# Optimization experiments

Measured on AMD Instinct MI355X. Metric: run time of the kernel, lower is better.

## Reference

```python
import jax, jax.numpy as jnp
import numpy as np

BN_EPS = 1e-5

def _bn(h, g, b):
    # BatchNorm1d training-mode math: biased batch stats over the node axis.
    m = h.mean(axis=0)
    v = h.var(axis=0)
    return (h - m) * jax.lax.rsqrt(v + BN_EPS) * g + b

def setup_inputs() -> dict:
    key = jax.random.key(0)
    ks = jax.random.split(key, 8)
    N, E, D_IN, H, L = 50000, 800000, 128, 256, 3
    return {
        "x": jax.random.normal(ks[0], (N, D_IN), dtype=jnp.float32),
        "edge_index": jax.random.randint(ks[1], (2, E), 0, N, dtype=jnp.int64),
        "eps": jnp.zeros((L,), dtype=jnp.float32),
        "W1_0": jax.random.normal(ks[2], (D_IN, H), dtype=jnp.float32),
        "W1_rest": jax.random.normal(ks[3], (L - 1, H, H), dtype=jnp.float32),
        "b1": jnp.zeros((L, H), dtype=jnp.float32),
        "g1": jnp.ones((L, H), dtype=jnp.float32),
        "bt1": jnp.zeros((L, H), dtype=jnp.float32),
        "W2": jax.random.normal(ks[4], (L, H, H), dtype=jnp.float32),
        "b2": jnp.zeros((L, H), dtype=jnp.float32),
        "g2": jnp.ones((L, H), dtype=jnp.float32),
        "bt2": jnp.zeros((L, H), dtype=jnp.float32),
    }

def reference(x, edge_index, eps, W1_0, W1_rest, b1, g1, bt1, W2, b2, g2, bt2):
    N = x.shape[0]
    row, col = edge_index[0], edge_index[1]
    L = eps.shape[0]

    def gin_layer(h, eps_i, Wa, ba, ga, bta, Wb, bb, gb, btb):
        # sum_{u in N(v)} h_u : gather source feats, scatter-add to dest rows
        agg = jax.ops.segment_sum(h[col], row, num_segments=N)
        out = (1.0 + eps_i) * h + agg
        out = _bn(out @ Wa + ba, ga, bta)        # Linear -> BN
        out = jax.nn.relu(out)                    # ReLU
        out = _bn(out @ Wb + bb, gb, btb)        # Linear -> BN
        return out

    h = x
    for i in range(L):
        Wa = W1_0 if i == 0 else W1_rest[i - 1]
        h = gin_layer(h, eps[i], Wa, b1[i], g1[i], bt1[i], W2[i], b2[i], g2[i], bt2[i])
        if i < L - 1:
            h = jax.nn.relu(h)  # inter-layer ReLU; dropout is identity in eval mode
    return h
```

## Files before the change

### kernel.cpp

```cpp
#include <hip/hip_runtime.h>
#include <hip/hip_bf16.h>
#include <math.h>
#include <stdint.h>

typedef short short8 __attribute__((ext_vector_type(8)));
typedef float f32x4 __attribute__((ext_vector_type(4)));

__device__ __forceinline__ float bf2f(unsigned int u) {
    union { unsigned int i; float f; } x; x.i = u << 16; return x.f;
}
__device__ __forceinline__ unsigned short f2bf(float f) {
    union { float f; unsigned int i; } x; x.f = f;
    unsigned int r = x.i + 0x7fffu + ((x.i >> 16) & 1u);
    return (unsigned short)(r >> 16);
}

__global__ void block_sums(const int* __restrict__ deg, int* __restrict__ bs, int N) {
    __shared__ int tmp[256];
    int t = threadIdx.x;
    int i = blockIdx.x * 256 + t;
    tmp[t] = (i < N) ? deg[i] : 0;
    __syncthreads();
    for (int off = 128; off > 0; off >>= 1) {
        if (t < off) tmp[t] += tmp[t + off];
        __syncthreads();
    }
    if (t == 0) bs[blockIdx.x] = tmp[0];
}
__global__ void scan_bs(const int* __restrict__ bs, int* __restrict__ bo, int B) {
    __shared__ int tmp[256];
    int t = threadIdx.x;
    int v = (t < B) ? bs[t] : 0;
    tmp[t] = v;
    __syncthreads();
    for (int off = 1; off < 256; off <<= 1) {
        int x = (t >= off) ? tmp[t - off] : 0;
        __syncthreads();
        tmp[t] += x;
        __syncthreads();
    }
    bo[t] = tmp[t] - v;
}
__global__ void finalize_rowptr(const int* __restrict__ deg, const int* __restrict__ bo,
                                int* __restrict__ rowptr, int* __restrict__ cursor,
                                int N, int E) {
    __shared__ int tmp[256];
    int t = threadIdx.x;
    int i = blockIdx.x * 256 + t;
    int v = (i < N) ? deg[i] : 0;
    tmp[t] = v;
    __syncthreads();
    for (int off = 1; off < 256; off <<= 1) {
        int x = (t >= off) ? tmp[t - off] : 0;
        __syncthreads();
        tmp[t] += x;
        __syncthreads();
    }
    int excl = tmp[t] - v + bo[blockIdx.x];
    if (i < N) { rowptr[i] = excl; cursor[i] = excl; }
    if (i == N) rowptr[N] = E;
}
__global__ void fill_csr(const int* __restrict__ row, const int* __restrict__ col,
                         int* __restrict__ cursor, int* __restrict__ idx, int E) {
    int e = blockIdx.x * blockDim.x + threadIdx.x;
    if (e < E) {
        int p = atomicAdd(&cursor[row[e]], 1);
        idx[p] = col[e];
    }
}

__global__ void zero_all(int* __restrict__ deg, int n_deg,
                         uint4* __restrict__ a, uint4* __restrict__ b, uint4* __restrict__ c,
                         int n_t, uint4* __restrict__ st, int n_st) {
    int i = blockIdx.x * blockDim.x + threadIdx.x;
    uint4 z = make_uint4(0, 0, 0, 0);
    if (i < n_deg) deg[i] = 0;
    if (i < n_t) { a[i] = z; b[i] = z; c[i] = z; }
    if (i < n_st) st[i] = z;
}

__global__ void prep_all(const float* __restrict__ x, unsigned short* __restrict__ xb, int nconv,
                         const float* __restrict__ W1_0, const float* __restrict__ W1rest,
                         const float* __restrict__ W2, unsigned short* __restrict__ wt,
                         const int* __restrict__ erow, int* __restrict__ deg, int E) {
    int i = blockIdx.x * blockDim.x + threadIdx.x;
    if (i < nconv) {
        float4 v = *(const float4*)(x + (size_t)i * 4);
        unsigned int lo = (unsigned int)f2bf(v.x) | ((unsigned int)f2bf(v.y) << 16);
        unsigned int hi = (unsigned int)f2bf(v.z) | ((unsigned int)f2bf(v.w) << 16);
        *(uint2*)(xb + (size_t)i * 4) = make_uint2(lo, hi);
        return;
    }
    int id = i - nconv;
    if (id < 32768) {
        int k = id >> 8, c = id & 255;
        wt[c * 128 + k] = f2bf(W1_0[id]);
        return;
    } else if (id < 163840) {
        int t = id - 32768;
        int m = t >> 16, r = t & 65535;
        int k = r >> 8, c = r & 255;
        wt[32768 + m * 65536 + c * 256 + k] = f2bf(W1rest[t]);
        return;
    } else if (id < 360448) {
        int t = id - 163840;
        int m = t >> 16, r = t & 65535;
        int k = r >> 8, c = r & 255;
        wt[163840 + m * 65536 + c * 256 + k] = f2bf(W2[t]);
        return;
    }
    int e = id - 360448;
    if (e < E) atomicAdd(&deg[erow[e]], 1);
}

template<int H, bool FUSE_BN>
__global__ __launch_bounds__(256) void aggregate_f(
    const unsigned short* __restrict__ h,
    const int* __restrict__ rowptr, const int* __restrict__ idx,
    const float* __restrict__ eps_p, int layer,
    const float* __restrict__ stats, const float* __restrict__ g,
    const float* __restrict__ bt, float invN,
    unsigned short* __restrict__ out, int N) {
    constexpr int NW = H / 128;
    int lane = threadIdx.x & 63;
    int v = blockIdx.x * 4 + (threadIdx.x >> 6);
    if (v >= N) return;

    float sc[2 * NW], sh[2 * NW];
    if constexpr (FUSE_BN) {
#pragma unroll
        for (int j = 0; j < 2 * NW; ++j) {
            int c = lane * 2 * NW + j;
            float m = stats[c] * invN;
            float var = stats[256 + c] * invN - m * m;
            sc[j] = g[c] * rsqrtf(var + 1e-5f);
            sh[j] = bt[c] - m * sc[j];
        }
    }
    const float s = 1.f + eps_p[layer];
    const unsigned int* hu = (const unsigned int*)h;

    float acc[2 * NW];
    {
        const unsigned int* hv = hu + (size_t)v * (H / 2) + lane * NW;
#pragma unroll
        for (int j = 0; j < NW; ++j) {
            unsigned int r = hv[j];
            float f0 = bf2f(r & 0xffffu), f1 = bf2f(r >> 16);
            if constexpr (FUSE_BN) {
                f0 = fmaxf(f0 * sc[2 * j] + sh[2 * j], 0.f);
                f1 = fmaxf(f1 * sc[2 * j + 1] + sh[2 * j + 1], 0.f);
            }
            acc[2 * j] = s * f0;
            acc[2 * j + 1] = s * f1;
        }
    }
    int e = rowptr[v], end = rowptr[v + 1];
    for (; e + 3 < end; e += 4) {
        int u0 = idx[e], u1 = idx[e + 1], u2 = idx[e + 2], u3 = idx[e + 3];
        const unsigned int* q0 = hu + (size_t)u0 * (H / 2) + lane * NW;
        const unsigned int* q1 = hu + (size_t)u1 * (H / 2) + lane * NW;
        const unsigned int* q2 = hu + (size_t)u2 * (H / 2) + lane * NW;
        const unsigned int* q3 = hu + (size_t)u3 * (H / 2) + lane * NW;
        unsigned int r0[NW], r1[NW], r2[NW], r3[NW];
#pragma unroll
        for (int j = 0; j < NW; ++j) { r0[j] = q0[j]; r1[j] = q1[j]; r2[j] = q2[j]; r3[j] = q3[j]; }
#pragma unroll
        for (int j = 0; j < NW; ++j) {
            float a0 = bf2f(r0[j] & 0xffffu), b0 = bf2f(r0[j] >> 16);
            float a1 = bf2f(r1[j] & 0xffffu), b1 = bf2f(r1[j] >> 16);
            float a2 = bf2f(r2[j] & 0xffffu), b2 = bf2f(r2[j] >> 16);
            float a3 = bf2f(r3[j] & 0xffffu), b3 = bf2f(r3[j] >> 16);
            if constexpr (FUSE_BN) {
                float c0 = sc[2 * j], d0 = sh[2 * j], c1 = sc[2 * j + 1], d1 = sh[2 * j + 1];
                a0 = fmaxf(a0 * c0 + d0, 0.f); b0 = fmaxf(b0 * c1 + d1, 0.f);
                a1 = fmaxf(a1 * c0 + d0, 0.f); b1 = fmaxf(b1 * c1 + d1, 0.f);
                a2 = fmaxf(a2 * c0 + d0, 0.f); b2 = fmaxf(b2 * c1 + d1, 0.f);
                a3 = fmaxf(a3 * c0 + d0, 0.f); b3 = fmaxf(b3 * c1 + d1, 0.f);
            }
            acc[2 * j]     += (a0 + a1) + (a2 + a3);
            acc[2 * j + 1] += (b0 + b1) + (b2 + b3);
        }
    }
    for (; e < end; ++e) {
        const unsigned int* q = hu + (size_t)idx[e] * (H / 2) + lane * NW;
#pragma unroll
        for (int j = 0; j < NW; ++j) {
            unsigned int r = q[j];
            float f0 = bf2f(r & 0xffffu), f1 = bf2f(r >> 16);
            if constexpr (FUSE_BN) {
                f0 = fmaxf(f0 * sc[2 * j] + sh[2 * j], 0.f);
                f1 = fmaxf(f1 * sc[2 * j + 1] + sh[2 * j + 1], 0.f);
            }
            acc[2 * j] += f0;
            acc[2 * j + 1] += f1;
        }
    }
    unsigned int* op = (unsigned int*)out + (size_t)v * (H / 2) + lane * NW;
#pragma unroll
    for (int j = 0; j < NW; ++j)
        op[j] = (unsigned int)f2bf(acc[2 * j]) | ((unsigned int)f2bf(acc[2 * j + 1]) << 16);
}

template<int K, bool TRANS_A>
__global__ __launch_bounds__(512, 4) void gemm_mfma(const unsigned short* __restrict__ A,
                                                 const unsigned short* __restrict__ Wt,
                                                 const float* __restrict__ bias,
                                                 const float* __restrict__ stats_in,
                                                 const float* __restrict__ gp,
                                                 const float* __restrict__ btp,
                                                 float invN,
                                                 unsigned short* __restrict__ Y,
                                                 float* __restrict__ stats_out,
                                                 int Nrows) {
    __shared__ unsigned short sA[2][128 * 32];
    __shared__ unsigned short sB[2][256 * 32];
    __shared__ float reds[256], redq[256];
    __shared__ float spc[256], sps[256];
    const int tid = threadIdx.x;
    const int lane = tid & 63;
    const int wid = tid >> 6;
    const int wm = wid >> 2;
    const int wn = wid & 3;
    const int r0 = blockIdx.x * 128;
    const int arow = tid >> 2;
    const int akk = (((tid & 3) ^ ((tid >> 3) & 3))) * 8;

    if constexpr (TRANS_A) {
        if (tid < 256) {
            float m = stats_in[tid] * invN;
            float var = stats_in[256 + tid] * invN - m * m;
            float sv = gp[tid] * rsqrtf(var + 1e-5f);
            spc[tid] = sv;
            sps[tid] = btp[tid] - m * sv;
        }
        __syncthreads();
    }

    f32x4 acc[4][4] = {};

    auto stageB = [&](int buf, int k0) {
#pragma unroll
        for (int q = 0; q < 2; ++q) {
            int row = q * 128 + arow;
            const unsigned short* gB = Wt + (size_t)row * K + k0 + akk;
            __builtin_amdgcn_global_load_lds(
                (const __attribute__((address_space(1))) void*)(uintptr_t)gB,
                (__attribute__((address_space(3))) void*)(uintptr_t)(&sB[buf][q * 4096 + tid * 8]),
                16, 0, 0);
        }
    };
    auto stageA_direct = [&](int buf, int k0) {
        const unsigned short* gA = A + (size_t)(r0 + arow) * K + k0 + akk;
        __builtin_amdgcn_global_load_lds(
            (const __attribute__((address_space(1))) void*)(uintptr_t)gA,
            (__attribute__((address_space(3))) void*)(uintptr_t)(&sA[buf][tid * 8]),
            16, 0, 0);
    };
    uint4 areg;
    auto loadA = [&](int k0) {
        areg = *(const uint4*)(A + (size_t)(r0 + arow) * K + k0 + akk);
    };
    auto writeA = [&](int buf, int k0) {
        float4 sca = *(const float4*)&spc[k0 + akk];
        float4 scb = *(const float4*)&spc[k0 + akk + 4];
        float4 sha = *(const float4*)&sps[k0 + akk];
        float4 shb = *(const float4*)&sps[k0 + akk + 4];
        uint4 u = areg;
        float f0 = fmaxf(bf2f(u.x & 0xffffu) * sca.x + sha.x, 0.f);
        float f1 = fmaxf(bf2f(u.x >> 16)     * sca.y + sha.y, 0.f);
        float f2 = fmaxf(bf2f(u.y & 0xffffu) * sca.z + sha.z, 0.f);
        float f3 = fmaxf(bf2f(u.y >> 16)     * sca.w + sha.w, 0.f);
        float f4 = fmaxf(bf2f(u.z & 0xffffu) * scb.x + shb.x, 0.f);
        float f5 = fmaxf(bf2f(u.z >> 16)     * scb.y + shb.y, 0.f);
        float f6 = fmaxf(bf2f(u.w & 0xffffu) * scb.z + shb.z, 0.f);
        float f7 = fmaxf(bf2f(u.w >> 16)     * scb.w + shb.w, 0.f);
        uint4 w;
        w.x = (unsigned int)f2bf(f0) | ((unsigned int)f2bf(f1) << 16);
        w.y = (unsigned int)f2bf(f2) | ((unsigned int)f2bf(f3) << 16);
        w.z = (unsigned int)f2bf(f4) | ((unsigned int)f2bf(f5) << 16);
        w.w = (unsigned int)f2bf(f6) | ((unsigned int)f2bf(f7) << 16);
        *(uint4*)&sA[buf][tid * 8] = w;
    };

    const int nt = K / 32;
    if constexpr (TRANS_A) { loadA(0); } else { stageA_direct(0, 0); }
    stageB(0, 0);
    const int krow = lane >> 4;
    const int rl = lane & 15;
    const int ksw = (rl >> 1) & 3;

    for (int t = 0; t < nt; ++t) {
        if constexpr (TRANS_A) writeA(t & 1, t * 32);
        __syncthreads();
        if (t + 1 < nt) {
            stageB((t + 1) & 1, (t + 1) * 32);
            if constexpr (TRANS_A) loadA((t + 1) * 32);
            else stageA_direct((t + 1) & 1, (t + 1) * 32);
        }
        const unsigned short* sAb = sA[t & 1];
        const unsigned short* sBb = sB[t & 1];
        short8 a[4], b[4];
#pragma unroll
        for (int i = 0; i < 4; ++i) {
            a[i] = *(const short8*)(sAb + (wm * 64 + i * 16 + rl) * 32 + (krow ^ ksw) * 8);
            b[i] = *(const short8*)(sBb + (wn * 64 + i * 16 + rl) * 32 + (krow ^ ksw) * 8);
        }
#pragma unroll
        for (int i = 0; i < 4; ++i)
#pragma unroll
            for (int n = 0; n < 4; ++n)
                asm volatile("v_mfma_f32_16x16x32_bf16 %0, %1, %2, %0"
                             : "+v"(acc[i][n])
                             : "v"(a[i]), "v"(b[n]));
    }
    asm volatile("s_nop 7\n\ts_nop 7" ::);

    const int rg = lane >> 4;
    float ssum[4], qsum[4];
#pragma unroll
    for (int n = 0; n < 4; ++n) {
        int col = wn * 64 + n * 16 + rl;
        float bvv = bias[col];
        float s = 0.f, q2 = 0.f;
#pragma unroll
        for (int i = 0; i < 4; ++i) {
#pragma unroll
            for (int r = 0; r < 4; ++r) {
                int grow = r0 + wm * 64 + i * 16 + rg * 4 + r;
                if (grow < Nrows) {
                    float v = acc[i][n][r] + bvv;
                    Y[(size_t)grow * 256 + col] = f2bf(v);
                    s += v;
                    q2 += v * v;
                }
            }
        }
        s  += __shfl_xor(s, 16, 64);  s  += __shfl_xor(s, 32, 64);
        q2 += __shfl_xor(q2, 16, 64); q2 += __shfl_xor(q2, 32, 64);
        ssum[n] = s; qsum[n] = q2;
    }
    if (wm == 0 && rg == 0) {
#pragma unroll
        for (int n = 0; n < 4; ++n) {
            int lc = wn * 64 + n * 16 + rl;
            reds[lc] = ssum[n];
            redq[lc] = qsum[n];
        }
    }
    __syncthreads();
    if (wm == 1 && rg == 0) {
#pragma unroll
        for (int n = 0; n < 4; ++n) {
            int lc = wn * 64 + n * 16 + rl;
            atomicAdd(&stats_out[lc], ssum[n] + reds[lc]);
            atomicAdd(&stats_out[256 + lc], qsum[n] + redq[lc]);
        }
    }
}

__global__ void bn_fuse(const unsigned short* __restrict__ Y, const float* __restrict__ stats,
                        const float* __restrict__ g, const float* __restrict__ bt,
                        float invN, float* __restrict__ outf, int total8) {
    int i = blockIdx.x * blockDim.x + threadIdx.x;
    if (i >= total8) return;
    int col0 = (i & 31) << 3;
    uint4 y = ((const uint4*)Y)[i];
    unsigned int yy[4] = {y.x, y.y, y.z, y.w};
    float o[8];
#pragma unroll
    for (int j = 0; j < 4; ++j) {
        o[2 * j]     = bf2f(yy[j] & 0xffffu);
        o[2 * j + 1] = bf2f(yy[j] >> 16);
    }
#pragma unroll
    for (int j = 0; j < 8; ++j) {
        int c = col0 + j;
        float mean = stats[c] * invN;
        float var = stats[256 + c] * invN - mean * mean;
        float sc = g[c] * rsqrtf(var + 1e-5f);
        float sh = bt[c] - mean * sc;
        o[j] = o[j] * sc + sh;
    }
    float4* of = (float4*)outf;
    of[2 * i]     = make_float4(o[0], o[1], o[2], o[3]);
    of[2 * i + 1] = make_float4(o[4], o[5], o[6], o[7]);
}

extern "C" void kernel_launch(void* const* d_in, const int* in_sizes, int n_in,
                              void* d_out, int out_size, void* d_ws, size_t ws_size,
                              hipStream_t stream) {
    const float* x      = (const float*)d_in[0];
    const int*   ei     = (const int*)d_in[1];
    const float* eps    = (const float*)d_in[2];
    const float* W1_0   = (const float*)d_in[3];
    const float* W1rest = (const float*)d_in[4];
    const float* b1     = (const float*)d_in[5];
    const float* g1     = (const float*)d_in[6];
    const float* bt1    = (const float*)d_in[7];
    const float* W2     = (const float*)d_in[8];
    const float* b2     = (const float*)d_in[9];
    const float* g2     = (const float*)d_in[10];
    const float* bt2    = (const float*)d_in[11];

    const int N = in_sizes[0] / 128;
    const int E = in_sizes[1] / 2;
    const int* row = ei;
    const int* col = ei + E;
    const int Npad = ((N + 127) / 128) * 128;
    const int nbRow = Npad / 128;

    char* w = (char*)d_ws;
    auto alloc = [&](size_t bytes) {
        char* p = w;
        w += (bytes + 255) & ~(size_t)255;
        return p;
    };
    unsigned short* xb = (unsigned short*)alloc((size_t)Npad * 128 * 2);
    unsigned short* p0 = (unsigned short*)alloc((size_t)Npad * 256 * 2);
    unsigned short* p1 = (unsigned short*)alloc((size_t)Npad * 256 * 2);
    unsigned short* Yb = (unsigned short*)alloc((size_t)Npad * 256 * 2);
    unsigned short* wt = (unsigned short*)alloc((size_t)360448 * 2);
    float* stats  = (float*)alloc(3072 * 4);
    int* deg    = (int*)alloc((size_t)N * 4);
    int* cursor = (int*)alloc((size_t)N * 4);
    int* rowptr = (int*)alloc((size_t)(N + 1) * 4);
    int* bs     = (int*)alloc(256 * 4);
    int* bo     = (int*)alloc(256 * 4);
    int* idxb   = (int*)alloc((size_t)E * 4);

    const float invN = 1.f / (float)N;
    const int B = (N + 255) / 256;

    int tail16 = (Npad - N) * 256 * 2 / 16;
    {
        uint4* t0 = (uint4*)(p0 + (size_t)N * 256);
        uint4* t1 = (uint4*)(p1 + (size_t)N * 256);
        uint4* t2 = (uint4*)(Yb + (size_t)N * 256);
        int mx = N;
        if (tail16 > mx) mx = tail16;
        if (768 > mx) mx = 768;
        zero_all<<<(mx + 255) / 256, 256, 0, stream>>>(deg, N, t0, t1, t2, tail16,
                                                       (uint4*)stats, 768);
    }

    const int nconv = N * 32;
    {
        int total = nconv + 360448 + E;
        prep_all<<<(total + 255) / 256, 256, 0, stream>>>(x, xb, nconv,
                                                          W1_0, W1rest, W2, wt,
                                                          row, deg, E);
    }

    block_sums<<<B, 256, 0, stream>>>(deg, bs, N);
    scan_bs<<<1, 256, 0, stream>>>(bs, bo, B);
    finalize_rowptr<<<B, 256, 0, stream>>>(deg, bo, rowptr, cursor, N, E);
    fill_csr<<<(E + 255) / 256, 256, 0, stream>>>(row, col, cursor, idxb, E);

    const int aggGrid = (N + 3) / 4;
    const int bnGrid = (N * 32 + 255) / 256;

    for (int layer = 0; layer < 3; ++layer) {
        float* st1 = stats + layer * 1024;
        float* st2 = st1 + 512;
        float* st2p = stats + (layer - 1) * 1024 + 512;

        if (layer == 0)
            aggregate_f<128, false><<<aggGrid, 256, 0, stream>>>(
                xb, rowptr, idxb, eps, 0, nullptr, nullptr, nullptr, invN, p1, N);
        else
            aggregate_f<256, true><<<aggGrid, 256, 0, stream>>>(
                p0, rowptr, idxb, eps, layer, st2p,
                g2 + (layer - 1) * 256, bt2 + (layer - 1) * 256, invN, p1, N);

        if (layer == 0)
            gemm_mfma<128, false><<<nbRow, 512, 0, stream>>>(
                p1, wt, b1, nullptr, nullptr, nullptr, invN, Yb, st1, N);
        else
            gemm_mfma<256, false><<<nbRow, 512, 0, stream>>>(
                p1, wt + 32768 + (size_t)(layer - 1) * 65536, b1 + layer * 256,
                nullptr, nullptr, nullptr, invN, Yb, st1, N);

        gemm_mfma<256, true><<<nbRow, 512, 0, stream>>>(
            Yb, wt + 163840 + (size_t)layer * 65536, b2 + layer * 256,
            st1, g1 + layer * 256, bt1 + layer * 256, invN, p0, st2, N);
    }

    bn_fuse<<<bnGrid, 256, 0, stream>>>(p0, stats + 2 * 1024 + 512,
                                        g2 + 2 * 256, bt2 + 2 * 256,
                                        invN, (float*)d_out, N * 32);
}
```

Measured before the change: 435.0 us.

## Merge CSR build and paired GEMMs into cooperative kernels with grid sync

Replaces the four CSR-construction launches with one cooperative kernel that uses grid-wide syncs between the block-sum, scan, rowptr and fill phases. Also fuses the two per-layer GEMMs into one cooperative persistent kernel (grid capped at 256 blocks) that loops over row strips, grid-syncs once the first GEMM's BN statistics are complete, and then runs the BN-fused second GEMM. The aim is to cut kernel launch overhead and inter-kernel gaps. In exchange, the GEMM grid is now limited to 256 persistent blocks, which may lower occupancy or load balance. Both paths keep the old launches as a fallback if the cooperative launch fails.

```diff
diff --git a/kernel.cpp b/kernel.cpp
--- a/kernel.cpp
+++ b/kernel.cpp
@@ -1,7 +1,10 @@
 #include <hip/hip_runtime.h>
 #include <hip/hip_bf16.h>
+#include <hip/hip_cooperative_groups.h>
 #include <math.h>
 #include <stdint.h>
+
+namespace cg = cooperative_groups;
 
 typedef short short8 __attribute__((ext_vector_type(8)));
 typedef float f32x4 __attribute__((ext_vector_type(4)));
@@ -13,60 +16,6 @@
     union { float f; unsigned int i; } x; x.f = f;
     unsigned int r = x.i + 0x7fffu + ((x.i >> 16) & 1u);
     return (unsigned short)(r >> 16);
-}
-
-__global__ void block_sums(const int* __restrict__ deg, int* __restrict__ bs, int N) {
-    __shared__ int tmp[256];
-    int t = threadIdx.x;
-    int i = blockIdx.x * 256 + t;
-    tmp[t] = (i < N) ? deg[i] : 0;
-    __syncthreads();
-    for (int off = 128; off > 0; off >>= 1) {
-        if (t < off) tmp[t] += tmp[t + off];
-        __syncthreads();
-    }
-    if (t == 0) bs[blockIdx.x] = tmp[0];
-}
-__global__ void scan_bs(const int* __restrict__ bs, int* __restrict__ bo, int B) {
-    __shared__ int tmp[256];
-    int t = threadIdx.x;
-    int v = (t < B) ? bs[t] : 0;
-    tmp[t] = v;
-    __syncthreads();
-    for (int off = 1; off < 256; off <<= 1) {
-        int x = (t >= off) ? tmp[t - off] : 0;
-        __syncthreads();
-        tmp[t] += x;
-        __syncthreads();
-    }
-    bo[t] = tmp[t] - v;
-}
-__global__ void finalize_rowptr(const int* __restrict__ deg, const int* __restrict__ bo,
-                                int* __restrict__ rowptr, int* __restrict__ cursor,
-                                int N, int E) {
-    __shared__ int tmp[256];
-    int t = threadIdx.x;
-    int i = blockIdx.x * 256 + t;
-    int v = (i < N) ? deg[i] : 0;
-    tmp[t] = v;
-    __syncthreads();
-    for (int off = 1; off < 256; off <<= 1) {
-        int x = (t >= off) ? tmp[t - off] : 0;
-        __syncthreads();
-        tmp[t] += x;
-        __syncthreads();
-    }
-    int excl = tmp[t] - v + bo[blockIdx.x];
-    if (i < N) { rowptr[i] = excl; cursor[i] = excl; }
-    if (i == N) rowptr[N] = E;
-}
-__global__ void fill_csr(const int* __restrict__ row, const int* __restrict__ col,
-                         int* __restrict__ cursor, int* __restrict__ idx, int E) {
-    int e = blockIdx.x * blockDim.x + threadIdx.x;
-    if (e < E) {
-        int p = atomicAdd(&cursor[row[e]], 1);
-        idx[p] = col[e];
-    }
 }
 
 __global__ void zero_all(int* __restrict__ deg, int n_deg,
@@ -113,6 +62,117 @@
     if (e < E) atomicAdd(&deg[erow[e]], 1);
 }
 
+__global__ void block_sums(const int* __restrict__ deg, int* __restrict__ bs, int N) {
+    __shared__ int tmp[256];
+    int t = threadIdx.x;
+    int i = blockIdx.x * 256 + t;
+    tmp[t] = (i < N) ? deg[i] : 0;
+    __syncthreads();
+    for (int off = 128; off > 0; off >>= 1) {
+        if (t < off) tmp[t] += tmp[t + off];
+        __syncthreads();
+    }
+    if (t == 0) bs[blockIdx.x] = tmp[0];
+}
+__global__ void scan_bs(const int* __restrict__ bs, int* __restrict__ bo, int B) {
+    __shared__ int tmp[256];
+    int t = threadIdx.x;
+    int v = (t < B) ? bs[t] : 0;
+    tmp[t] = v;
+    __syncthreads();
+    for (int off = 1; off < 256; off <<= 1) {
+        int x = (t >= off) ? tmp[t - off] : 0;
+        __syncthreads();
+        tmp[t] += x;
+        __syncthreads();
+    }
+    bo[t] = tmp[t] - v;
+}
+__global__ void finalize_rowptr(const int* __restrict__ deg, const int* __restrict__ bo,
+                                int* __restrict__ rowptr, int* __restrict__ cursor,
+                                int N, int E) {
+    __shared__ int tmp[256];
+    int t = threadIdx.x;
+    int i = blockIdx.x * 256 + t;
+    int v = (i < N) ? deg[i] : 0;
+    tmp[t] = v;
+    __syncthreads();
+    for (int off = 1; off < 256; off <<= 1) {
+        int x = (t >= off) ? tmp[t - off] : 0;
+        __syncthreads();
+        tmp[t] += x;
+        __syncthreads();
+    }
+    int excl = tmp[t] - v + bo[blockIdx.x];
+    if (i < N) { rowptr[i] = excl; cursor[i] = excl; }
+    if (i == N) rowptr[N] = E;
+}
+__global__ void fill_csr(const int* __restrict__ row, const int* __restrict__ col,
+                         int* __restrict__ cursor, int* __restrict__ idx, int E) {
+    int e = blockIdx.x * blockDim.x + threadIdx.x;
+    if (e < E) {
+        int p = atomicAdd(&cursor[row[e]], 1);
+        idx[p] = col[e];
+    }
+}
+
+__global__ __launch_bounds__(256) void csr_coop(const int* __restrict__ deg,
+                                                int* __restrict__ bs, int* __restrict__ bo,
+                                                int* __restrict__ rowptr, int* __restrict__ cursor,
+                                                const int* __restrict__ row, const int* __restrict__ col,
+                                                int* __restrict__ idx, int N, int E) {
+    cg::grid_group grid = cg::this_grid();
+    __shared__ int tmp[256];
+    const int t = threadIdx.x;
+    const int b = blockIdx.x;
+    {
+        int i = b * 256 + t;
+        tmp[t] = (i < N) ? deg[i] : 0;
+        __syncthreads();
+        for (int off = 128; off > 0; off >>= 1) {
+            if (t < off) tmp[t] += tmp[t + off];
+            __syncthreads();
+        }
+        if (t == 0) bs[b] = tmp[0];
+    }
+    grid.sync();
+    if (b == 0) {
+        int B = gridDim.x;
+        int v = (t < B) ? bs[t] : 0;
+        tmp[t] = v;
+        __syncthreads();
+        for (int off = 1; off < 256; off <<= 1) {
+            int x = (t >= off) ? tmp[t - off] : 0;
+            __syncthreads();
+            tmp[t] += x;
+            __syncthreads();
+        }
+        bo[t] = tmp[t] - v;
+    }
+    grid.sync();
+    {
+        int i = b * 256 + t;
+        int v = (i < N) ? deg[i] : 0;
+        tmp[t] = v;
+        __syncthreads();
+        for (int off = 1; off < 256; off <<= 1) {
+            int x = (t >= off) ? tmp[t - off] : 0;
+            __syncthreads();
+            tmp[t] += x;
+            __syncthreads();
+        }
+        int excl = tmp[t] - v + bo[b];
+        if (i < N) { rowptr[i] = excl; cursor[i] = excl; }
+        if (i == N) rowptr[N] = E;
+    }
+    grid.sync();
+    int gid = b * 256 + t, gsz = gridDim.x * 256;
+    for (int e = gid; e < E; e += gsz) {
+        int p = atomicAdd(&cursor[row[e]], 1);
+        idx[p] = col[e];
+    }
+}
+
 template<int H, bool FUSE_BN>
 __global__ __launch_bounds__(256) void aggregate_f(
     const unsigned short* __restrict__ h,
@@ -202,40 +262,39 @@
         op[j] = (unsigned int)f2bf(acc[2 * j]) | ((unsigned int)f2bf(acc[2 * j + 1]) << 16);
 }
 
+struct GemmLds {
+    unsigned short sA[2][128 * 32];
+    unsigned short sB[2][256 * 32];
+    float reds[256], redq[256];
+    float spc[256], sps[256];
+};
+
+__device__ __forceinline__ void bn_params_to_lds(GemmLds& L, const float* stats_in,
+                                                 const float* gp, const float* btp,
+                                                 float invN) {
+    int tid = threadIdx.x;
+    if (tid < 256) {
+        float m = stats_in[tid] * invN;
+        float var = stats_in[256 + tid] * invN - m * m;
+        float sv = gp[tid] * rsqrtf(var + 1e-5f);
+        L.spc[tid] = sv;
+        L.sps[tid] = btp[tid] - m * sv;
+    }
+    __syncthreads();
+}
+
 template<int K, bool TRANS_A>
-__global__ __launch_bounds__(512, 4) void gemm_mfma(const unsigned short* __restrict__ A,
-                                                 const unsigned short* __restrict__ Wt,
-                                                 const float* __restrict__ bias,
-                                                 const float* __restrict__ stats_in,
-                                                 const float* __restrict__ gp,
-                                                 const float* __restrict__ btp,
-                                                 float invN,
-                                                 unsigned short* __restrict__ Y,
-                                                 float* __restrict__ stats_out,
-                                                 int Nrows) {
-    __shared__ unsigned short sA[2][128 * 32];
-    __shared__ unsigned short sB[2][256 * 32];
-    __shared__ float reds[256], redq[256];
-    __shared__ float spc[256], sps[256];
+__device__ __forceinline__ void gemm_strip(GemmLds& L, int r0,
+    const unsigned short* __restrict__ A, const unsigned short* __restrict__ Wt,
+    const float* __restrict__ bias, unsigned short* __restrict__ Y,
+    float* __restrict__ stats_out, int Nrows) {
     const int tid = threadIdx.x;
     const int lane = tid & 63;
     const int wid = tid >> 6;
     const int wm = wid >> 2;
     const int wn = wid & 3;
-    const int r0 = blockIdx.x * 128;
     const int arow = tid >> 2;
     const int akk = (((tid & 3) ^ ((tid >> 3) & 3))) * 8;
-
-    if constexpr (TRANS_A) {
-        if (tid < 256) {
-            float m = stats_in[tid] * invN;
-            float var = stats_in[256 + tid] * invN - m * m;
-            float sv = gp[tid] * rsqrtf(var + 1e-5f);
-            spc[tid] = sv;
-            sps[tid] = btp[tid] - m * sv;
-        }
-        __syncthreads();
-    }
 
     f32x4 acc[4][4] = {};
 
@@ -246,7 +305,7 @@
             const unsigned short* gB = Wt + (size_t)row * K + k0 + akk;
             __builtin_amdgcn_global_load_lds(
                 (const __attribute__((address_space(1))) void*)(uintptr_t)gB,
-                (__attribute__((address_space(3))) void*)(uintptr_t)(&sB[buf][q * 4096 + tid * 8]),
+                (__attribute__((address_space(3))) void*)(uintptr_t)(&L.sB[buf][q * 4096 + tid * 8]),
                 16, 0, 0);
         }
     };
@@ -254,7 +313,7 @@
         const unsigned short* gA = A + (size_t)(r0 + arow) * K + k0 + akk;
         __builtin_amdgcn_global_load_lds(
             (const __attribute__((address_space(1))) void*)(uintptr_t)gA,
-            (__attribute__((address_space(3))) void*)(uintptr_t)(&sA[buf][tid * 8]),
+            (__attribute__((address_space(3))) void*)(uintptr_t)(&L.sA[buf][tid * 8]),
             16, 0, 0);
     };
     uint4 areg;
@@ -262,10 +321,10 @@
         areg = *(const uint4*)(A + (size_t)(r0 + arow) * K + k0 + akk);
     };
     auto writeA = [&](int buf, int k0) {
-        float4 sca = *(const float4*)&spc[k0 + akk];
-        float4 scb = *(const float4*)&spc[k0 + akk + 4];
-        float4 sha = *(const float4*)&sps[k0 + akk];
-        float4 shb = *(const float4*)&sps[k0 + akk + 4];
+        float4 sca = *(const float4*)&L.spc[k0 + akk];
+        float4 scb = *(const float4*)&L.spc[k0 + akk + 4];
+        float4 sha = *(const float4*)&L.sps[k0 + akk];
+        float4 shb = *(const float4*)&L.sps[k0 + akk + 4];
         uint4 u = areg;
         float f0 = fmaxf(bf2f(u.x & 0xffffu) * sca.x + sha.x, 0.f);
         float f1 = fmaxf(bf2f(u.x >> 16)     * sca.y + sha.y, 0.f);
@@ -280,7 +339,7 @@
         w.y = (unsigned int)f2bf(f2) | ((unsigned int)f2bf(f3) << 16);
         w.z = (unsigned int)f2bf(f4) | ((unsigned int)f2bf(f5) << 16);
         w.w = (unsigned int)f2bf(f6) | ((unsigned int)f2bf(f7) << 16);
-        *(uint4*)&sA[buf][tid * 8] = w;
+        *(uint4*)&L.sA[buf][tid * 8] = w;
     };
 
     const int nt = K / 32;
@@ -298,8 +357,8 @@
             if constexpr (TRANS_A) loadA((t + 1) * 32);
             else stageA_direct((t + 1) & 1, (t + 1) * 32);
         }
-        const unsigned short* sAb = sA[t & 1];
-        const unsigned short* sBb = sB[t & 1];
+        const unsigned short* sAb = L.sA[t & 1];
+        const unsigned short* sBb = L.sB[t & 1];
         short8 a[4], b[4];
 #pragma unroll
         for (int i = 0; i < 4; ++i) {
@@ -344,8 +403,8 @@
 #pragma unroll
         for (int n = 0; n < 4; ++n) {
             int lc = wn * 64 + n * 16 + rl;
-            reds[lc] = ssum[n];
-            redq[lc] = qsum[n];
+            L.reds[lc] = ssum[n];
+            L.redq[lc] = qsum[n];
         }
     }
     __syncthreads();
@@ -353,10 +412,44 @@
 #pragma unroll
         for (int n = 0; n < 4; ++n) {
             int lc = wn * 64 + n * 16 + rl;
-            atomicAdd(&stats_out[lc], ssum[n] + reds[lc]);
-            atomicAdd(&stats_out[256 + lc], qsum[n] + redq[lc]);
-        }
-    }
+            atomicAdd(&stats_out[lc], ssum[n] + L.reds[lc]);
+            atomicAdd(&stats_out[256 + lc], qsum[n] + L.redq[lc]);
+        }
+    }
+}
+
+template<int K, bool TRANS_A>
+__global__ __launch_bounds__(512, 4) void gemm_mfma(const unsigned short* __restrict__ A,
+                                                    const unsigned short* __restrict__ Wt,
+                                                    const float* __restrict__ bias,
+                                                    const float* __restrict__ stats_in,
+                                                    const float* __restrict__ gp,
+                                                    const float* __restrict__ btp,
+                                                    float invN,
+                                                    unsigned short* __restrict__ Y,
+                                                    float* __restrict__ stats_out,
+                                                    int Nrows) {
+    __shared__ GemmLds L;
+    if constexpr (TRANS_A) bn_params_to_lds(L, stats_in, gp, btp, invN);
+    gemm_strip<K, TRANS_A>(L, blockIdx.x * 128, A, Wt, bias, Y, stats_out, Nrows);
+}
+
+template<int K1>
+__global__ __launch_bounds__(512, 4) void gemm_pair(
+    const unsigned short* __restrict__ A1, const unsigned short* __restrict__ Wt1,
+    const float* __restrict__ bias1, unsigned short* __restrict__ Y1,
+    float* __restrict__ st1,
+    const unsigned short* __restrict__ Wt2, const float* __restrict__ bias2,
+    const float* __restrict__ g1p, const float* __restrict__ bt1p,
+    float invN, unsigned short* __restrict__ Y2, float* __restrict__ st2,
+    int Nrows, int nStrips) {
+    __shared__ GemmLds L;
+    for (int s = blockIdx.x; s < nStrips; s += gridDim.x)
+        gemm_strip<K1, false>(L, s * 128, A1, Wt1, bias1, Y1, st1, Nrows);
+    cg::this_grid().sync();
+    bn_params_to_lds(L, st1, g1p, bt1p, invN);
+    for (int s = blockIdx.x; s < nStrips; s += gridDim.x)
+        gemm_strip<256, true>(L, s * 128, Y1, Wt2, bias2, Y2, st2, Nrows);
 }
 
 __global__ void bn_fuse(const unsigned short* __restrict__ Y, const float* __restrict__ stats,
@@ -452,13 +545,25 @@
                                                           row, deg, E);
     }
 
-    block_sums<<<B, 256, 0, stream>>>(deg, bs, N);
-    scan_bs<<<1, 256, 0, stream>>>(bs, bo, B);
-    finalize_rowptr<<<B, 256, 0, stream>>>(deg, bo, rowptr, cursor, N, E);
-    fill_csr<<<(E + 255) / 256, 256, 0, stream>>>(row, col, cursor, idxb, E);
+    {
+        const int* degc = deg;
+        int Nv = N, Ev = E;
+        void* args[] = {(void*)&degc, (void*)&bs, (void*)&bo, (void*)&rowptr,
+                        (void*)&cursor, (void*)&row, (void*)&col, (void*)&idxb,
+                        (void*)&Nv, (void*)&Ev};
+        hipError_t err = hipLaunchCooperativeKernel((const void*)csr_coop, dim3(B),
+                                                    dim3(256), args, 0, stream);
+        if (err != hipSuccess) {
+            block_sums<<<B, 256, 0, stream>>>(deg, bs, N);
+            scan_bs<<<1, 256, 0, stream>>>(bs, bo, B);
+            finalize_rowptr<<<B, 256, 0, stream>>>(deg, bo, rowptr, cursor, N, E);
+            fill_csr<<<(E + 255) / 256, 256, 0, stream>>>(row, col, cursor, idxb, E);
+        }
+    }
 
     const int aggGrid = (N + 3) / 4;
     const int bnGrid = (N * 32 + 255) / 256;
+    const int coopGrid = nbRow < 256 ? nbRow : 256;
 
     for (int layer = 0; layer < 3; ++layer) {
         float* st1 = stats + layer * 1024;
@@ -473,17 +578,38 @@
                 p0, rowptr, idxb, eps, layer, st2p,
                 g2 + (layer - 1) * 256, bt2 + (layer - 1) * 256, invN, p1, N);
 
-        if (layer == 0)
-            gemm_mfma<128, false><<<nbRow, 512, 0, stream>>>(
-                p1, wt, b1, nullptr, nullptr, nullptr, invN, Yb, st1, N);
-        else
-            gemm_mfma<256, false><<<nbRow, 512, 0, stream>>>(
-                p1, wt + 32768 + (size_t)(layer - 1) * 65536, b1 + layer * 256,
-                nullptr, nullptr, nullptr, invN, Yb, st1, N);
-
-        gemm_mfma<256, true><<<nbRow, 512, 0, stream>>>(
-            Yb, wt + 163840 + (size_t)layer * 65536, b2 + layer * 256,
-            st1, g1 + layer * 256, bt1 + layer * 256, invN, p0, st2, N);
+        const unsigned short* A1  = p1;
+        const unsigned short* Wt1 = (layer == 0) ? wt
+                                    : wt + 32768 + (size_t)(layer - 1) * 65536;
+        const float* b1l  = b1 + layer * 256;
+        unsigned short* Y1 = Yb;
+        float* s1 = st1;
+        const unsigned short* Wt2 = wt + 163840 + (size_t)layer * 65536;
+        const float* b2l  = b2 + layer * 256;
+        const float* g1l  = g1 + layer * 256;
+        const float* bt1l = bt1 + layer * 256;
+        float invNv = invN;
+        unsigned short* Y2 = p0;
+        float* s2 = st2;
+        int Nr = N, nS = nbRow;
+        void* args[] = {(void*)&A1, (void*)&Wt1, (void*)&b1l, (void*)&Y1,
+                        (void*)&s1, (void*)&Wt2, (void*)&b2l, (void*)&g1l,
+                        (void*)&bt1l, (void*)&invNv, (void*)&Y2, (void*)&s2,
+                        (void*)&Nr, (void*)&nS};
+        const void* kfn = (layer == 0) ? (const void*)gemm_pair<128>
+                                       : (const void*)gemm_pair<256>;
+        hipError_t err = hipLaunchCooperativeKernel(kfn, dim3(coopGrid), dim3(512),
+                                                    args, 0, stream);
+        if (err != hipSuccess) {
+            if (layer == 0)
+                gemm_mfma<128, false><<<nbRow, 512, 0, stream>>>(
+                    A1, Wt1, b1l, nullptr, nullptr, nullptr, invN, Y1, s1, N);
+            else
+                gemm_mfma<256, false><<<nbRow, 512, 0, stream>>>(
+                    A1, Wt1, b1l, nullptr, nullptr, nullptr, invN, Y1, s1, N);
+            gemm_mfma<256, true><<<nbRow, 512, 0, stream>>>(
+                Y1, Wt2, b2l, s1, g1l, bt1l, invN, Y2, s2, N);
+        }
     }
 
     bn_fuse<<<bnGrid, 256, 0, stream>>>(p0, stats + 2 * 1024 + 512,
```

New measurement: 723.0 us. 1.66x slower.
